# Optimization experiments

Hardware: AMD Instinct MI355X
Metric: run time of the kernel (lower is better)

Reference implementation:

```python
import jax, jax.numpy as jnp
import numpy as np

B, L, D = 4096, 50, 64
U, V, R = 100000, 100000, 5

def _lin(key, fan_out, fan_in):
    kw, kb = jax.random.split(key)
    s = 1.0 / np.sqrt(fan_in)
    return (jax.random.uniform(kw, (fan_out, fan_in), jnp.float32, -s, s),
            jax.random.uniform(kb, (fan_out,), jnp.float32, -s, s))

def setup_inputs() -> dict:
    key = jax.random.key(0)
    ks = jax.random.split(key, 12)
    w_r1_w, w_r1_b = _lin(ks[0], D, 2 * D)
    w_r2_w, w_r2_b = _lin(ks[1], D, D)
    att1_w, att1_b = _lin(ks[2], D, 2 * D)
    att2_w, att2_b = _lin(ks[3], D, D)
    att3_w, att3_b = _lin(ks[4], 1, D)
    return {
        "nodes": jax.random.randint(ks[5], (B,), 0, U),
        "history_uv": jax.random.randint(ks[6], (B, L), 0, V),
        "history_r": jax.random.randint(ks[7], (B, L), 0, R),
        "history_uvt": jax.random.randint(ks[8], (B, L), 0, 512),
        "v2e_w": jax.random.normal(ks[9], (V, D), jnp.float32) * 0.05,
        "u2e_w": jax.random.normal(ks[10], (U, D), jnp.float32) * 0.05,
        "r2e_w": jax.random.normal(ks[11], (R, D), jnp.float32) * 0.05,
        "w_r1_w": w_r1_w, "w_r1_b": w_r1_b,
        "w_r2_w": w_r2_w, "w_r2_b": w_r2_b,
        "att1_w": att1_w, "att1_b": att1_b,
        "att2_w": att2_w, "att2_b": att2_b,
        "att3_w": att3_w, "att3_b": att3_b,
    }

def reference(nodes, history_uv, history_r, history_uvt,
              v2e_w, u2e_w, r2e_w,
              w_r1_w, w_r1_b, w_r2_w, w_r2_b,
              att1_w, att1_b, att2_w, att2_b, att3_w, att3_b):
    # Gathers (uv=True branch): item embeddings for neighbor history, user rep for node
    e_uv = v2e_w[history_uv]          # (B, L, D)
    e_r = r2e_w[history_r]            # (B, L, D)
    uv_rep = u2e_w[nodes]             # (B, D)
    # Two-layer MLP on [e_uv ; e_r]
    x = jnp.concatenate([e_uv, e_r], axis=-1)               # (B, L, 2D)
    h = jax.nn.relu(jnp.einsum('blk,dk->bld', x, w_r1_w) + w_r1_b)
    o = jax.nn.relu(jnp.einsum('blk,dk->bld', h, w_r2_w) + w_r2_b)  # (B, L, D)
    # GraphRec Attention: MLP([o ; uv_rep]) -> scalar -> softmax over neighbors
    uv_b = jnp.broadcast_to(uv_rep[:, None, :], o.shape)     # (B, L, D)
    xa = jnp.concatenate([o, uv_b], axis=-1)                 # (B, L, 2D)
    a = jax.nn.relu(jnp.einsum('blk,dk->bld', xa, att1_w) + att1_b)
    a = jax.nn.relu(jnp.einsum('blk,dk->bld', a, att2_w) + att2_b)
    s = jnp.einsum('bld,od->blo', a, att3_w)[..., 0] + att3_b[0]    # (B, L)
    w = jax.nn.softmax(s, axis=1)                            # softmax over neighbors
    # att_history = o^T @ att_w  per node
    out = jnp.einsum('bld,bl->bd', o, w)                     # (B, D)
    return out
```

## Files before the change

### kernel.cpp

```cpp
#include <hip/hip_runtime.h>


#define LNB 50

typedef _Float16 f16x8 __attribute__((ext_vector_type(8)));
typedef float    f32x4 __attribute__((ext_vector_type(4)));

__device__ __forceinline__ int swz(int r, int bytecol) {
  return (r * 128 + bytecol) ^ ((r & 7) << 4);
}

__device__ __forceinline__ f16x8 cvt8(const float* __restrict__ p) {
  const float4 lo = *(const float4*)p;
  const float4 hi = *(const float4*)(p + 4);
  f16x8 a;
  a[0] = (_Float16)lo.x; a[1] = (_Float16)lo.y;
  a[2] = (_Float16)lo.z; a[3] = (_Float16)lo.w;
  a[4] = (_Float16)hi.x; a[5] = (_Float16)hi.y;
  a[6] = (_Float16)hi.z; a[7] = (_Float16)hi.w;
  return a;
}

__global__ void prep_weights(const float* __restrict__ w1, const float* __restrict__ w2,
                             const float* __restrict__ a1, const float* __restrict__ a2,
                             _Float16* __restrict__ wf) {
  int i = blockIdx.x * 256 + threadIdx.x;
  if (i < 8192) wf[i]         = (_Float16)w1[i];
  if (i < 4096) wf[8192 + i]  = (_Float16)w2[i];
  if (i < 8192) wf[12288 + i] = (_Float16)a1[i];
  if (i < 4096) wf[20480 + i] = (_Float16)a2[i];
}

__global__ __launch_bounds__(64, 2) void uvagg_fused(
    const int* __restrict__ nodes,
    const int* __restrict__ hist_uv,
    const int* __restrict__ hist_r,
    const float* __restrict__ v2e,
    const float* __restrict__ u2e,
    const float* __restrict__ r2e,
    const float* __restrict__ b1,
    const float* __restrict__ b2,
    const float* __restrict__ ab1,
    const float* __restrict__ ab2,
    const float* __restrict__ a3w,
    const _Float16* __restrict__ wf,
    float* __restrict__ out) {
  __shared__ _Float16 T[64 * 64];
  __shared__ float scb[64];
  __shared__ float wtb[64];
  const int lane = threadIdx.x;
  const int lr = lane & 15;
  const int kq = lane >> 4;
  const int b = blockIdx.x;

  const _Float16* w1f = wf;
  const _Float16* w2f = wf + 8192;
  const _Float16* a1f = wf + 12288;
  const _Float16* a2f = wf + 20480;

  {
    f16x8 Bf[4][4];
#pragma unroll
    for (int kt = 0; kt < 4; ++kt)
#pragma unroll
      for (int nt = 0; nt < 4; ++nt)
        Bf[kt][nt] = *(const f16x8*)(w1f + (nt * 16 + lr) * 128 + kt * 32 + kq * 8);

    float bias1[4];
#pragma unroll
    for (int nt = 0; nt < 4; ++nt) bias1[nt] = b1[nt * 16 + lr];

#pragma unroll
    for (int m = 0; m < 4; ++m) {
      const int rr = b * LNB + (m * 16 + lr < LNB ? m * 16 + lr : LNB - 1);
      const int iu = hist_uv[rr];
      const int ir = hist_r[rr];
      const float* pu = v2e + (size_t)iu * 64;
      const float* pr = r2e + (size_t)ir * 64;
      f16x8 A[4];
      A[0] = cvt8(pu + kq * 8);
      A[1] = cvt8(pu + 32 + kq * 8);
      A[2] = cvt8(pr + kq * 8);
      A[3] = cvt8(pr + 32 + kq * 8);
#pragma unroll
      for (int nt = 0; nt < 4; ++nt) {
        f32x4 acc = {0.f, 0.f, 0.f, 0.f};
#pragma unroll
        for (int kt = 0; kt < 4; ++kt)
          acc = __builtin_amdgcn_mfma_f32_16x16x32_f16(A[kt], Bf[kt][nt], acc, 0, 0, 0);
        const int c = nt * 16 + lr;
#pragma unroll
        for (int j = 0; j < 4; ++j) {
          const int row = m * 16 + kq * 4 + j;
          const float v = fmaxf(acc[j] + bias1[nt], 0.f);
          *(_Float16*)((char*)T + swz(row, 2 * c)) = (_Float16)v;
        }
      }
    }
  }
  __syncthreads();

  f16x8 HA0[4], HA1[4];
#pragma unroll
  for (int m = 0; m < 4; ++m) {
    const int r = m * 16 + lr;
    HA0[m] = *(const f16x8*)((char*)T + swz(r, 2 * (kq * 8)));
    HA1[m] = *(const f16x8*)((char*)T + swz(r, 2 * (32 + kq * 8)));
  }
  __syncthreads();

  {
    f16x8 Bf[2][4];
#pragma unroll
    for (int kt = 0; kt < 2; ++kt)
#pragma unroll
      for (int nt = 0; nt < 4; ++nt)
        Bf[kt][nt] = *(const f16x8*)(w2f + (nt * 16 + lr) * 64 + kt * 32 + kq * 8);

    float bias2[4];
#pragma unroll
    for (int nt = 0; nt < 4; ++nt) bias2[nt] = b2[nt * 16 + lr];

#pragma unroll
    for (int m = 0; m < 4; ++m) {
#pragma unroll
      for (int nt = 0; nt < 4; ++nt) {
        f32x4 acc = {0.f, 0.f, 0.f, 0.f};
        acc = __builtin_amdgcn_mfma_f32_16x16x32_f16(HA0[m], Bf[0][nt], acc, 0, 0, 0);
        acc = __builtin_amdgcn_mfma_f32_16x16x32_f16(HA1[m], Bf[1][nt], acc, 0, 0, 0);
        const int c = nt * 16 + lr;
#pragma unroll
        for (int j = 0; j < 4; ++j) {
          const int row = m * 16 + kq * 4 + j;
          const float v = fmaxf(acc[j] + bias2[nt], 0.f);
          *(_Float16*)((char*)T + swz(row, 2 * c)) = (_Float16)v;
        }
      }
    }
  }
  __syncthreads();

  f16x8 OA0[4], OA1[4];
#pragma unroll
  for (int m = 0; m < 4; ++m) {
    const int r = m * 16 + lr;
    OA0[m] = *(const f16x8*)((char*)T + swz(r, 2 * (kq * 8)));
    OA1[m] = *(const f16x8*)((char*)T + swz(r, 2 * (32 + kq * 8)));
  }
  __syncthreads();

  {
    const int node = nodes[b];
    f32x4 acc_u[4];
    {
      f16x8 Bu[2][4];
#pragma unroll
      for (int kt = 0; kt < 2; ++kt)
#pragma unroll
        for (int nt = 0; nt < 4; ++nt)
          Bu[kt][nt] = *(const f16x8*)(a1f + (nt * 16 + lr) * 128 + (kt + 2) * 32 + kq * 8);
      const f16x8 U2 = cvt8(u2e + (size_t)node * 64 + kq * 8);
      const f16x8 U3 = cvt8(u2e + (size_t)node * 64 + 32 + kq * 8);
#pragma unroll
      for (int nt = 0; nt < 4; ++nt) {
        f32x4 acc = {0.f, 0.f, 0.f, 0.f};
        acc = __builtin_amdgcn_mfma_f32_16x16x32_f16(U2, Bu[0][nt], acc, 0, 0, 0);
        acc = __builtin_amdgcn_mfma_f32_16x16x32_f16(U3, Bu[1][nt], acc, 0, 0, 0);
        acc_u[nt] = acc;
      }
    }

    f16x8 Bf[2][4];
#pragma unroll
    for (int kt = 0; kt < 2; ++kt)
#pragma unroll
      for (int nt = 0; nt < 4; ++nt)
        Bf[kt][nt] = *(const f16x8*)(a1f + (nt * 16 + lr) * 128 + kt * 32 + kq * 8);

    float biasa1[4];
#pragma unroll
    for (int nt = 0; nt < 4; ++nt) biasa1[nt] = ab1[nt * 16 + lr];

#pragma unroll
    for (int m = 0; m < 4; ++m) {
#pragma unroll
      for (int nt = 0; nt < 4; ++nt) {
        f32x4 acc = acc_u[nt];
        acc = __builtin_amdgcn_mfma_f32_16x16x32_f16(OA0[m], Bf[0][nt], acc, 0, 0, 0);
        acc = __builtin_amdgcn_mfma_f32_16x16x32_f16(OA1[m], Bf[1][nt], acc, 0, 0, 0);
        const int c = nt * 16 + lr;
#pragma unroll
        for (int j = 0; j < 4; ++j) {
          const int row = m * 16 + kq * 4 + j;
          const float v = fmaxf(acc[j] + biasa1[nt], 0.f);
          *(_Float16*)((char*)T + swz(row, 2 * c)) = (_Float16)v;
        }
      }
    }
  }
  __syncthreads();

  {
    f16x8 Bf[2][4];
#pragma unroll
    for (int kt = 0; kt < 2; ++kt)
#pragma unroll
      for (int nt = 0; nt < 4; ++nt)
        Bf[kt][nt] = *(const f16x8*)(a2f + (nt * 16 + lr) * 64 + kt * 32 + kq * 8);

    float biasa2[4], a3c[4];
#pragma unroll
    for (int nt = 0; nt < 4; ++nt) {
      biasa2[nt] = ab2[nt * 16 + lr];
      a3c[nt] = a3w[nt * 16 + lr];
    }

#pragma unroll
    for (int m = 0; m < 4; ++m) {
      const int r = m * 16 + lr;
      f16x8 A0  = *(const f16x8*)((char*)T + swz(r, 2 * (kq * 8)));
      f16x8 A1v = *(const f16x8*)((char*)T + swz(r, 2 * (32 + kq * 8)));
      float part[4] = {0.f, 0.f, 0.f, 0.f};
#pragma unroll
      for (int nt = 0; nt < 4; ++nt) {
        f32x4 acc = {0.f, 0.f, 0.f, 0.f};
        acc = __builtin_amdgcn_mfma_f32_16x16x32_f16(A0,  Bf[0][nt], acc, 0, 0, 0);
        acc = __builtin_amdgcn_mfma_f32_16x16x32_f16(A1v, Bf[1][nt], acc, 0, 0, 0);
#pragma unroll
        for (int j = 0; j < 4; ++j) {
          const float v = fmaxf(acc[j] + biasa2[nt], 0.f);
          part[j] += v * a3c[nt];
        }
      }
#pragma unroll
      for (int mask = 1; mask < 16; mask <<= 1)
#pragma unroll
        for (int j = 0; j < 4; ++j) part[j] += __shfl_xor(part[j], mask);
      if (lr == 0) {
#pragma unroll
        for (int j = 0; j < 4; ++j) scb[m * 16 + kq * 4 + j] = part[j];
      }
    }
  }
  __syncthreads();

  {
    float sv = (lane < LNB) ? scb[lane] : -1e30f;
    float mx = sv;
#pragma unroll
    for (int mask = 1; mask < 64; mask <<= 1) mx = fmaxf(mx, __shfl_xor(mx, mask));
    const float e = __expf(sv - mx);
    float s = e;
#pragma unroll
    for (int mask = 1; mask < 64; mask <<= 1) s += __shfl_xor(s, mask);
    wtb[lane] = (lane < LNB) ? (e / s) : 0.f;
  }
  __syncthreads();

  {
    float wrow[4];
#pragma unroll
    for (int m = 0; m < 4; ++m) wrow[m] = wtb[m * 16 + lr];

    float p0[8] = {0,0,0,0,0,0,0,0};
    float p1[8] = {0,0,0,0,0,0,0,0};
#pragma unroll
    for (int m = 0; m < 4; ++m)
#pragma unroll
      for (int i = 0; i < 8; ++i) {
        p0[i] += wrow[m] * (float)OA0[m][i];
        p1[i] += wrow[m] * (float)OA1[m][i];
      }
#pragma unroll
    for (int mask = 1; mask < 16; mask <<= 1)
#pragma unroll
      for (int i = 0; i < 8; ++i) {
        p0[i] += __shfl_xor(p0[i], mask);
        p1[i] += __shfl_xor(p1[i], mask);
      }
    if (lr == 0) {
#pragma unroll
      for (int i = 0; i < 8; ++i) {
        scb[kq * 8 + i] = p0[i];
        scb[32 + kq * 8 + i] = p1[i];
      }
    }
  }
  __syncthreads();
  out[(size_t)b * 64 + lane] = scb[lane];
}

extern "C" void kernel_launch(void* const* d_in, const int* in_sizes, int n_in,
                              void* d_out, int out_size, void* d_ws, size_t ws_size,
                              hipStream_t stream) {
  (void)in_sizes; (void)n_in; (void)out_size; (void)ws_size;
  const int* nodes = (const int*)d_in[0];
  const int* huv   = (const int*)d_in[1];
  const int* hr    = (const int*)d_in[2];
  const float* v2e = (const float*)d_in[4];
  const float* u2e = (const float*)d_in[5];
  const float* r2e = (const float*)d_in[6];
  const float* w1  = (const float*)d_in[7];
  const float* b1  = (const float*)d_in[8];
  const float* w2  = (const float*)d_in[9];
  const float* b2  = (const float*)d_in[10];
  const float* a1  = (const float*)d_in[11];
  const float* ab1 = (const float*)d_in[12];
  const float* a2  = (const float*)d_in[13];
  const float* ab2 = (const float*)d_in[14];
  const float* a3  = (const float*)d_in[15];

  _Float16* wf = (_Float16*)d_ws;
  prep_weights<<<32, 256, 0, stream>>>(w1, w2, a1, a2, wf);
  uvagg_fused<<<4096, 64, 0, stream>>>(nodes, huv, hr, v2e, u2e, r2e,
                                       b1, b2, ab1, ab2, a3, wf,
                                       (float*)d_out);
}
```

Measured before the change: 155.7 us.

## Process two batch rows per wavefront to amortize weight fragment loads

Each 64-thread block now handles two batch elements instead of one, halving the grid to 2048 blocks. Weight fragments and biases loaded into registers are reused across both rows, and the two independent rows give more MFMA and memory-level parallelism within a wave. The cost is doubled LDS per block and much higher register pressure (HA/OA arrays doubled), which can cause spills or lower occupancy, and there are fewer blocks to spread across CUs.

```diff
diff --git a/kernel.cpp b/kernel.cpp
--- a/kernel.cpp
+++ b/kernel.cpp
@@ -31,7 +31,7 @@
   if (i < 4096) wf[20480 + i] = (_Float16)a2[i];
 }
 
-__global__ __launch_bounds__(64, 2) void uvagg_fused(
+__global__ __launch_bounds__(64, 2) void uvagg_fused2(
     const int* __restrict__ nodes,
     const int* __restrict__ hist_uv,
     const int* __restrict__ hist_r,
@@ -45,13 +45,13 @@
     const float* __restrict__ a3w,
     const _Float16* __restrict__ wf,
     float* __restrict__ out) {
-  __shared__ _Float16 T[64 * 64];
-  __shared__ float scb[64];
-  __shared__ float wtb[64];
+  __shared__ _Float16 T[2][64 * 64];
+  __shared__ float scb[2][64];
+  __shared__ float wtb[2][64];
   const int lane = threadIdx.x;
   const int lr = lane & 15;
   const int kq = lane >> 4;
-  const int b = blockIdx.x;
+  const int b0 = blockIdx.x * 2;
 
   const _Float16* w1f = wf;
   const _Float16* w2f = wf + 8192;
@@ -71,41 +71,49 @@
     for (int nt = 0; nt < 4; ++nt) bias1[nt] = b1[nt * 16 + lr];
 
 #pragma unroll
+    for (int q = 0; q < 2; ++q) {
+      char* Tq = (char*)T[q];
+#pragma unroll
+      for (int m = 0; m < 4; ++m) {
+        const int rr = (b0 + q) * LNB + (m * 16 + lr < LNB ? m * 16 + lr : LNB - 1);
+        const int iu = hist_uv[rr];
+        const int ir = hist_r[rr];
+        const float* pu = v2e + (size_t)iu * 64;
+        const float* pr = r2e + (size_t)ir * 64;
+        f16x8 A[4];
+        A[0] = cvt8(pu + kq * 8);
+        A[1] = cvt8(pu + 32 + kq * 8);
+        A[2] = cvt8(pr + kq * 8);
+        A[3] = cvt8(pr + 32 + kq * 8);
+#pragma unroll
+        for (int nt = 0; nt < 4; ++nt) {
+          f32x4 acc = {0.f, 0.f, 0.f, 0.f};
+#pragma unroll
+          for (int kt = 0; kt < 4; ++kt)
+            acc = __builtin_amdgcn_mfma_f32_16x16x32_f16(A[kt], Bf[kt][nt], acc, 0, 0, 0);
+          const int c = nt * 16 + lr;
+#pragma unroll
+          for (int j = 0; j < 4; ++j) {
+            const int row = m * 16 + kq * 4 + j;
+            const float v = fmaxf(acc[j] + bias1[nt], 0.f);
+            *(_Float16*)(Tq + swz(row, 2 * c)) = (_Float16)v;
+          }
+        }
+      }
+    }
+  }
+  __syncthreads();
+
+  f16x8 HA0[2][4], HA1[2][4];
+#pragma unroll
+  for (int q = 0; q < 2; ++q) {
+    const char* Tq = (const char*)T[q];
+#pragma unroll
     for (int m = 0; m < 4; ++m) {
-      const int rr = b * LNB + (m * 16 + lr < LNB ? m * 16 + lr : LNB - 1);
-      const int iu = hist_uv[rr];
-      const int ir = hist_r[rr];
-      const float* pu = v2e + (size_t)iu * 64;
-      const float* pr = r2e + (size_t)ir * 64;
-      f16x8 A[4];
-      A[0] = cvt8(pu + kq * 8);
-      A[1] = cvt8(pu + 32 + kq * 8);
-      A[2] = cvt8(pr + kq * 8);
-      A[3] = cvt8(pr + 32 + kq * 8);
-#pragma unroll
-      for (int nt = 0; nt < 4; ++nt) {
-        f32x4 acc = {0.f, 0.f, 0.f, 0.f};
-#pragma unroll
-        for (int kt = 0; kt < 4; ++kt)
-          acc = __builtin_amdgcn_mfma_f32_16x16x32_f16(A[kt], Bf[kt][nt], acc, 0, 0, 0);
-        const int c = nt * 16 + lr;
-#pragma unroll
-        for (int j = 0; j < 4; ++j) {
-          const int row = m * 16 + kq * 4 + j;
-          const float v = fmaxf(acc[j] + bias1[nt], 0.f);
-          *(_Float16*)((char*)T + swz(row, 2 * c)) = (_Float16)v;
-        }
-      }
-    }
-  }
-  __syncthreads();
-
-  f16x8 HA0[4], HA1[4];
-#pragma unroll
-  for (int m = 0; m < 4; ++m) {
-    const int r = m * 16 + lr;
-    HA0[m] = *(const f16x8*)((char*)T + swz(r, 2 * (kq * 8)));
-    HA1[m] = *(const f16x8*)((char*)T + swz(r, 2 * (32 + kq * 8)));
+      const int r = m * 16 + lr;
+      HA0[q][m] = *(const f16x8*)(Tq + swz(r, 2 * (kq * 8)));
+      HA1[q][m] = *(const f16x8*)(Tq + swz(r, 2 * (32 + kq * 8)));
+    }
   }
   __syncthreads();
 
@@ -122,36 +130,43 @@
     for (int nt = 0; nt < 4; ++nt) bias2[nt] = b2[nt * 16 + lr];
 
 #pragma unroll
+    for (int q = 0; q < 2; ++q) {
+      char* Tq = (char*)T[q];
+#pragma unroll
+      for (int m = 0; m < 4; ++m) {
+#pragma unroll
+        for (int nt = 0; nt < 4; ++nt) {
+          f32x4 acc = {0.f, 0.f, 0.f, 0.f};
+          acc = __builtin_amdgcn_mfma_f32_16x16x32_f16(HA0[q][m], Bf[0][nt], acc, 0, 0, 0);
+          acc = __builtin_amdgcn_mfma_f32_16x16x32_f16(HA1[q][m], Bf[1][nt], acc, 0, 0, 0);
+          const int c = nt * 16 + lr;
+#pragma unroll
+          for (int j = 0; j < 4; ++j) {
+            const int row = m * 16 + kq * 4 + j;
+            const float v = fmaxf(acc[j] + bias2[nt], 0.f);
+            *(_Float16*)(Tq + swz(row, 2 * c)) = (_Float16)v;
+          }
+        }
+      }
+    }
+  }
+  __syncthreads();
+
+  f16x8 OA0[2][4], OA1[2][4];
+#pragma unroll
+  for (int q = 0; q < 2; ++q) {
+    const char* Tq = (const char*)T[q];
+#pragma unroll
     for (int m = 0; m < 4; ++m) {
-#pragma unroll
-      for (int nt = 0; nt < 4; ++nt) {
-        f32x4 acc = {0.f, 0.f, 0.f, 0.f};
-        acc = __builtin_amdgcn_mfma_f32_16x16x32_f16(HA0[m], Bf[0][nt], acc, 0, 0, 0);
-        acc = __builtin_amdgcn_mfma_f32_16x16x32_f16(HA1[m], Bf[1][nt], acc, 0, 0, 0);
-        const int c = nt * 16 + lr;
-#pragma unroll
-        for (int j = 0; j < 4; ++j) {
-          const int row = m * 16 + kq * 4 + j;
-          const float v = fmaxf(acc[j] + bias2[nt], 0.f);
-          *(_Float16*)((char*)T + swz(row, 2 * c)) = (_Float16)v;
-        }
-      }
-    }
-  }
-  __syncthreads();
-
-  f16x8 OA0[4], OA1[4];
-#pragma unroll
-  for (int m = 0; m < 4; ++m) {
-    const int r = m * 16 + lr;
-    OA0[m] = *(const f16x8*)((char*)T + swz(r, 2 * (kq * 8)));
-    OA1[m] = *(const f16x8*)((char*)T + swz(r, 2 * (32 + kq * 8)));
-  }
-  __syncthreads();
-
-  {
-    const int node = nodes[b];
-    f32x4 acc_u[4];
+      const int r = m * 16 + lr;
+      OA0[q][m] = *(const f16x8*)(Tq + swz(r, 2 * (kq * 8)));
+      OA1[q][m] = *(const f16x8*)(Tq + swz(r, 2 * (32 + kq * 8)));
+    }
+  }
+  __syncthreads();
+
+  {
+    f32x4 acc_u[2][4];
     {
       f16x8 Bu[2][4];
 #pragma unroll
@@ -159,14 +174,18 @@
 #pragma unroll
         for (int nt = 0; nt < 4; ++nt)
           Bu[kt][nt] = *(const f16x8*)(a1f + (nt * 16 + lr) * 128 + (kt + 2) * 32 + kq * 8);
-      const f16x8 U2 = cvt8(u2e + (size_t)node * 64 + kq * 8);
-      const f16x8 U3 = cvt8(u2e + (size_t)node * 64 + 32 + kq * 8);
-#pragma unroll
-      for (int nt = 0; nt < 4; ++nt) {
-        f32x4 acc = {0.f, 0.f, 0.f, 0.f};
-        acc = __builtin_amdgcn_mfma_f32_16x16x32_f16(U2, Bu[0][nt], acc, 0, 0, 0);
-        acc = __builtin_amdgcn_mfma_f32_16x16x32_f16(U3, Bu[1][nt], acc, 0, 0, 0);
-        acc_u[nt] = acc;
+#pragma unroll
+      for (int q = 0; q < 2; ++q) {
+        const int node = nodes[b0 + q];
+        const f16x8 U2 = cvt8(u2e + (size_t)node * 64 + kq * 8);
+        const f16x8 U3 = cvt8(u2e + (size_t)node * 64 + 32 + kq * 8);
+#pragma unroll
+        for (int nt = 0; nt < 4; ++nt) {
+          f32x4 acc = {0.f, 0.f, 0.f, 0.f};
+          acc = __builtin_amdgcn_mfma_f32_16x16x32_f16(U2, Bu[0][nt], acc, 0, 0, 0);
+          acc = __builtin_amdgcn_mfma_f32_16x16x32_f16(U3, Bu[1][nt], acc, 0, 0, 0);
+          acc_u[q][nt] = acc;
+        }
       }
     }
 
@@ -182,18 +201,22 @@
     for (int nt = 0; nt < 4; ++nt) biasa1[nt] = ab1[nt * 16 + lr];
 
 #pragma unroll
-    for (int m = 0; m < 4; ++m) {
-#pragma unroll
-      for (int nt = 0; nt < 4; ++nt) {
-        f32x4 acc = acc_u[nt];
-        acc = __builtin_amdgcn_mfma_f32_16x16x32_f16(OA0[m], Bf[0][nt], acc, 0, 0, 0);
-        acc = __builtin_amdgcn_mfma_f32_16x16x32_f16(OA1[m], Bf[1][nt], acc, 0, 0, 0);
-        const int c = nt * 16 + lr;
-#pragma unroll
-        for (int j = 0; j < 4; ++j) {
-          const int row = m * 16 + kq * 4 + j;
-          const float v = fmaxf(acc[j] + biasa1[nt], 0.f);
-          *(_Float16*)((char*)T + swz(row, 2 * c)) = (_Float16)v;
+    for (int q = 0; q < 2; ++q) {
+      char* Tq = (char*)T[q];
+#pragma unroll
+      for (int m = 0; m < 4; ++m) {
+#pragma unroll
+        for (int nt = 0; nt < 4; ++nt) {
+          f32x4 acc = acc_u[q][nt];
+          acc = __builtin_amdgcn_mfma_f32_16x16x32_f16(OA0[q][m], Bf[0][nt], acc, 0, 0, 0);
+          acc = __builtin_amdgcn_mfma_f32_16x16x32_f16(OA1[q][m], Bf[1][nt], acc, 0, 0, 0);
+          const int c = nt * 16 + lr;
+#pragma unroll
+          for (int j = 0; j < 4; ++j) {
+            const int row = m * 16 + kq * 4 + j;
+            const float v = fmaxf(acc[j] + biasa1[nt], 0.f);
+            *(_Float16*)(Tq + swz(row, 2 * c)) = (_Float16)v;
+          }
         }
       }
     }
@@ -218,76 +241,104 @@
 #pragma unroll
     for (int m = 0; m < 4; ++m) {
       const int r = m * 16 + lr;
-      f16x8 A0  = *(const f16x8*)((char*)T + swz(r, 2 * (kq * 8)));
-      f16x8 A1v = *(const f16x8*)((char*)T + swz(r, 2 * (32 + kq * 8)));
-      float part[4] = {0.f, 0.f, 0.f, 0.f};
+      f16x8 A0q[2], A1q[2];
+#pragma unroll
+      for (int q = 0; q < 2; ++q) {
+        const char* Tq = (const char*)T[q];
+        A0q[q] = *(const f16x8*)(Tq + swz(r, 2 * (kq * 8)));
+        A1q[q] = *(const f16x8*)(Tq + swz(r, 2 * (32 + kq * 8)));
+      }
+      float part[2][4] = {{0.f,0.f,0.f,0.f},{0.f,0.f,0.f,0.f}};
 #pragma unroll
       for (int nt = 0; nt < 4; ++nt) {
-        f32x4 acc = {0.f, 0.f, 0.f, 0.f};
-        acc = __builtin_amdgcn_mfma_f32_16x16x32_f16(A0,  Bf[0][nt], acc, 0, 0, 0);
-        acc = __builtin_amdgcn_mfma_f32_16x16x32_f16(A1v, Bf[1][nt], acc, 0, 0, 0);
-#pragma unroll
-        for (int j = 0; j < 4; ++j) {
-          const float v = fmaxf(acc[j] + biasa2[nt], 0.f);
-          part[j] += v * a3c[nt];
+#pragma unroll
+        for (int q = 0; q < 2; ++q) {
+          f32x4 acc = {0.f, 0.f, 0.f, 0.f};
+          acc = __builtin_amdgcn_mfma_f32_16x16x32_f16(A0q[q], Bf[0][nt], acc, 0, 0, 0);
+          acc = __builtin_amdgcn_mfma_f32_16x16x32_f16(A1q[q], Bf[1][nt], acc, 0, 0, 0);
+#pragma unroll
+          for (int j = 0; j < 4; ++j) {
+            const float v = fmaxf(acc[j] + biasa2[nt], 0.f);
+            part[q][j] += v * a3c[nt];
+          }
         }
       }
 #pragma unroll
       for (int mask = 1; mask < 16; mask <<= 1)
 #pragma unroll
-        for (int j = 0; j < 4; ++j) part[j] += __shfl_xor(part[j], mask);
+        for (int q = 0; q < 2; ++q)
+#pragma unroll
+          for (int j = 0; j < 4; ++j) part[q][j] += __shfl_xor(part[q][j], mask);
       if (lr == 0) {
 #pragma unroll
-        for (int j = 0; j < 4; ++j) scb[m * 16 + kq * 4 + j] = part[j];
-      }
-    }
-  }
-  __syncthreads();
-
-  {
-    float sv = (lane < LNB) ? scb[lane] : -1e30f;
-    float mx = sv;
-#pragma unroll
-    for (int mask = 1; mask < 64; mask <<= 1) mx = fmaxf(mx, __shfl_xor(mx, mask));
-    const float e = __expf(sv - mx);
-    float s = e;
-#pragma unroll
-    for (int mask = 1; mask < 64; mask <<= 1) s += __shfl_xor(s, mask);
-    wtb[lane] = (lane < LNB) ? (e / s) : 0.f;
-  }
-  __syncthreads();
-
-  {
-    float wrow[4];
-#pragma unroll
-    for (int m = 0; m < 4; ++m) wrow[m] = wtb[m * 16 + lr];
-
-    float p0[8] = {0,0,0,0,0,0,0,0};
-    float p1[8] = {0,0,0,0,0,0,0,0};
-#pragma unroll
-    for (int m = 0; m < 4; ++m)
-#pragma unroll
-      for (int i = 0; i < 8; ++i) {
-        p0[i] += wrow[m] * (float)OA0[m][i];
-        p1[i] += wrow[m] * (float)OA1[m][i];
-      }
+        for (int q = 0; q < 2; ++q)
+#pragma unroll
+          for (int j = 0; j < 4; ++j) scb[q][m * 16 + kq * 4 + j] = part[q][j];
+      }
+    }
+  }
+  __syncthreads();
+
+  {
+    float sv[2], mx[2], e[2], s[2];
+#pragma unroll
+    for (int q = 0; q < 2; ++q) { sv[q] = (lane < LNB) ? scb[q][lane] : -1e30f; mx[q] = sv[q]; }
+#pragma unroll
+    for (int mask = 1; mask < 64; mask <<= 1)
+#pragma unroll
+      for (int q = 0; q < 2; ++q) mx[q] = fmaxf(mx[q], __shfl_xor(mx[q], mask));
+#pragma unroll
+    for (int q = 0; q < 2; ++q) { e[q] = __expf(sv[q] - mx[q]); s[q] = e[q]; }
+#pragma unroll
+    for (int mask = 1; mask < 64; mask <<= 1)
+#pragma unroll
+      for (int q = 0; q < 2; ++q) s[q] += __shfl_xor(s[q], mask);
+#pragma unroll
+    for (int q = 0; q < 2; ++q) wtb[q][lane] = (lane < LNB) ? (e[q] / s[q]) : 0.f;
+  }
+  __syncthreads();
+
+  {
+    float wrow[2][4];
+#pragma unroll
+    for (int q = 0; q < 2; ++q)
+#pragma unroll
+      for (int m = 0; m < 4; ++m) wrow[q][m] = wtb[q][m * 16 + lr];
+
+    float p0[2][8] = {{0,0,0,0,0,0,0,0},{0,0,0,0,0,0,0,0}};
+    float p1[2][8] = {{0,0,0,0,0,0,0,0},{0,0,0,0,0,0,0,0}};
+#pragma unroll
+    for (int q = 0; q < 2; ++q)
+#pragma unroll
+      for (int m = 0; m < 4; ++m)
+#pragma unroll
+        for (int i = 0; i < 8; ++i) {
+          p0[q][i] += wrow[q][m] * (float)OA0[q][m][i];
+          p1[q][i] += wrow[q][m] * (float)OA1[q][m][i];
+        }
 #pragma unroll
     for (int mask = 1; mask < 16; mask <<= 1)
 #pragma unroll
-      for (int i = 0; i < 8; ++i) {
-        p0[i] += __shfl_xor(p0[i], mask);
-        p1[i] += __shfl_xor(p1[i], mask);
-      }
+      for (int q = 0; q < 2; ++q)
+#pragma unroll
+        for (int i = 0; i < 8; ++i) {
+          p0[q][i] += __shfl_xor(p0[q][i], mask);
+          p1[q][i] += __shfl_xor(p1[q][i], mask);
+        }
     if (lr == 0) {
 #pragma unroll
-      for (int i = 0; i < 8; ++i) {
-        scb[kq * 8 + i] = p0[i];
-        scb[32 + kq * 8 + i] = p1[i];
-      }
-    }
-  }
-  __syncthreads();
-  out[(size_t)b * 64 + lane] = scb[lane];
+      for (int q = 0; q < 2; ++q)
+#pragma unroll
+        for (int i = 0; i < 8; ++i) {
+          scb[q][kq * 8 + i] = p0[q][i];
+          scb[q][32 + kq * 8 + i] = p1[q][i];
+        }
+    }
+  }
+  __syncthreads();
+#pragma unroll
+  for (int q = 0; q < 2; ++q)
+    out[(size_t)(b0 + q) * 64 + lane] = scb[q][lane];
 }
 
 extern "C" void kernel_launch(void* const* d_in, const int* in_sizes, int n_in,
@@ -312,7 +363,7 @@
 
   _Float16* wf = (_Float16*)d_ws;
   prep_weights<<<32, 256, 0, stream>>>(w1, w2, a1, a2, wf);
-  uvagg_fused<<<4096, 64, 0, stream>>>(nodes, huv, hr, v2e, u2e, r2e,
-                                       b1, b2, ab1, ab2, a3, wf,
-                                       (float*)d_out);
-}
+  uvagg_fused2<<<2048, 64, 0, stream>>>(nodes, huv, hr, v2e, u2e, r2e,
+                                        b1, b2, ab1, ab2, a3, wf,
+                                        (float*)d_out);
+}
```

After: 144.8 us. 1.08x faster.
